# Kernel optimization log

Hardware: AMD Instinct MI355X
Metric: run time of the kernel (lower is better)

The kernel has to match this reference:

```python
import jax, jax.numpy as jnp
import numpy as np

N_WIRES = 8
DIM = 1 << N_WIRES  # 256

# Precompute CNOT permutations (torchquantum convention: wire 0 = MSB)
_idx = np.arange(DIM)
_CNOT_PERMS = []
for _c in range(N_WIRES):
    _t = (_c + 1) % N_WIRES
    _cbit = (_idx >> (N_WIRES - 1 - _c)) & 1
    _CNOT_PERMS.append(np.where(_cbit == 1, _idx ^ (1 << (N_WIRES - 1 - _t)), _idx))
# PauliZ signs per wire: [DIM, N_WIRES]
_ZSIGNS = np.stack([1.0 - 2.0 * ((_idx >> (N_WIRES - 1 - w)) & 1) for w in range(N_WIRES)], axis=1).astype(np.float32)


def _quantum_heads(x, theta):
    """x: [B,S,H,8] angles; theta: [8]. Returns PauliZ expectations [B,S,H,8].

    Simulates per (token,head) an 8-qubit circuit: RX(x_i+theta_i) on wire i
    (encoder RX followed by trainable RX on same wire = one RX with summed angle),
    then CNOT ring 0->1..6->7, 7->0, then MeasureAll PauliZ.
    """
    B, S, H, _ = x.shape
    N = B * S * H
    ang = x.reshape(N, N_WIRES) + theta  # [N,8]
    state = jnp.zeros((N, DIM), dtype=jnp.complex64).at[:, 0].set(1.0)
    half = ang * 0.5
    c_all = jnp.cos(half)
    s_all = jnp.sin(half)
    for w in range(N_WIRES):
        A = 1 << w
        Bdim = 1 << (N_WIRES - 1 - w)
        s = state.reshape(N, A, 2, Bdim)
        a0, a1 = s[:, :, 0, :], s[:, :, 1, :]
        c = c_all[:, w][:, None, None].astype(jnp.complex64)
        isn = (1j * s_all[:, w][:, None, None]).astype(jnp.complex64)
        n0 = c * a0 - isn * a1
        n1 = -isn * a0 + c * a1
        state = jnp.stack([n0, n1], axis=2).reshape(N, DIM)
    for perm in _CNOT_PERMS:
        state = state[:, perm]
    probs = state.real ** 2 + state.imag ** 2  # [N,256]
    exp = probs @ jnp.asarray(_ZSIGNS)  # [N,8]
    return exp.reshape(B, S, H, N_WIRES)


def _mha(proj, W_combine, num_heads):
    # proj: [B,S,E]; q = k = v = proj (identical deterministic projections)
    B, S, E = proj.shape
    d_k = E // num_heads
    qkv = proj.reshape(B, S, num_heads, d_k).transpose(0, 2, 1, 3)  # [B,H,S,dk]
    scores = jnp.einsum('bhqd,bhkd->bhqk', qkv, qkv) / jnp.sqrt(jnp.float32(d_k))
    attn = jax.nn.softmax(scores, axis=-1)
    out = jnp.einsum('bhqk,bhkd->bhqd', attn, qkv)
    out = out.transpose(0, 2, 1, 3).reshape(B, S, E)
    return out @ W_combine.T


def setup_inputs() -> dict:
    key = jax.random.key(0)
    k1, k2, k3 = jax.random.split(key, 3)
    B, S, H = 8, 1024, 8
    E = H * N_WIRES  # 64
    x = jax.random.normal(k1, (B, S, E), dtype=jnp.float32)
    theta = jax.random.normal(k2, (N_WIRES,), dtype=jnp.float32)
    W_combine = jax.random.normal(k3, (E, E), dtype=jnp.float32) * (1.0 / np.sqrt(E))
    return {'x': x, 'theta': theta, 'W_combine': W_combine}


def reference(x, theta, W_combine):
    B, S, E = x.shape
    H = E // N_WIRES
    proj = _quantum_heads(x.reshape(B, S, H, N_WIRES), theta).reshape(B, S, E)
    return _mha(proj, W_combine, H)
```

## Files before the change

kernel.cpp:

```cpp
#include <hip/hip_runtime.h>

typedef _Float16 half4v __attribute__((ext_vector_type(4)));
typedef __fp16 fp16x2 __attribute__((ext_vector_type(2)));
typedef float float4v __attribute__((ext_vector_type(4)));

#define S_ 1024
#define H_ 8
#define B_ 8
#define BH 64
#define NROW 8192
#define E_ 64

#define VST 1032
#define VZOFF (9 * VST)
#define NV (9 * VST + 16)
#define KFZ (64 * 128)
#define NKF (64 * 128 + 8)

static __device__ inline half4v pack4(float a, float b, float c, float d) {
    union { fp16x2 f2[2]; half4v h4; } u;
    u.f2[0] = __builtin_amdgcn_cvt_pkrtz(a, b);
    u.f2[1] = __builtin_amdgcn_cvt_pkrtz(c, d);
    return u.h4;
}

__global__ __launch_bounds__(256, 2) void attn_kernel(
        const float* __restrict__ x, const float* __restrict__ theta,
        _Float16* __restrict__ attnH) {
    __shared__ _Float16 kF[NKF];
    __shared__ _Float16 vT[NV];
    int bh = blockIdx.x;
    int b = bh >> 3, h = bh & 7;
    int tid = threadIdx.x;

    float th[8];
#pragma unroll
    for (int i = 0; i < 8; ++i) th[i] = theta[i];

    {
        const half4v zer = {(_Float16)0.f, (_Float16)0.f, (_Float16)0.f, (_Float16)0.f};
        const half4v one = {(_Float16)1.f, (_Float16)1.f, (_Float16)1.f, (_Float16)1.f};
        if (tid < 4) *(half4v*)&vT[VZOFF + tid * 4] = zer;
        if (tid < 2) *(half4v*)&kF[KFZ + tid * 4] = zer;
        *(half4v*)&vT[8 * VST + tid * 4] = one;
    }

    for (int s = tid; s < S_; s += 256) {
        const float4* xp = (const float4*)(x + (((size_t)(b << 10) + s) << 6) + (h << 3));
        float4 x0 = xp[0];
        float4 x1 = xp[1];
        float c0 = __cosf(x0.x + th[0]);
        float c1 = __cosf(x0.y + th[1]);
        float c2 = __cosf(x0.z + th[2]);
        float c3 = __cosf(x0.w + th[3]);
        float c4 = __cosf(x1.x + th[4]);
        float c5 = __cosf(x1.y + th[5]);
        float c6 = __cosf(x1.z + th[6]);
        float c7 = __cosf(x1.w + th[7]);
        float e1 = c0 * c1;
        float e2 = e1 * c2;
        float e3 = e2 * c3;
        float e4 = e3 * c4;
        float e5 = e4 * c5;
        float e6 = e5 * c6;
        float e7 = e6 * c7;
        float e0 = ((c1 * c2) * (c3 * c4)) * ((c5 * c6) * c7);
        half4v lo = pack4(e0, e1, e2, e3);
        half4v hi = pack4(e4, e5, e6, e7);
        int kt = s >> 4, c = s & 15;
        *(half4v*)&kF[kt * 128 + c * 4]      = lo;
        *(half4v*)&kF[kt * 128 + 64 + c * 4] = hi;
        vT[0 * VST + s] = lo[0]; vT[1 * VST + s] = lo[1];
        vT[2 * VST + s] = lo[2]; vT[3 * VST + s] = lo[3];
        vT[4 * VST + s] = hi[0]; vT[5 * VST + s] = hi[1];
        vT[6 * VST + s] = hi[2]; vT[7 * VST + s] = hi[3];
    }
    __syncthreads();

    int lane = tid & 63;
    int wv   = tid >> 6;
    int col  = lane & 15;
    int quad = lane >> 4;
    int q0   = blockIdx.y * 128 + wv * 32;

    bool lo2 = (quad < 2);

    int kfa = lo2 ? (lane * 4) : KFZ;
    int kstep = lo2 ? 128 : 0;

    half4v qfa = *(const half4v*)&kF[kfa + (q0 >> 4) * kstep];
    half4v qfb = *(const half4v*)&kF[kfa + ((q0 >> 4) + 1) * kstep];
    qfa *= (_Float16)0.51012921f;
    qfb *= (_Float16)0.51012921f;

    int vbase = (col < 9) ? (col * VST + quad * 4) : VZOFF;
    int vstep = (col < 9) ? 16 : 0;

#define LOADK(dst, t) { dst = *(const half4v*)&kF[kfa + (t) * kstep]; }
#define LOADV(dst, t) { dst = *(const half4v*)&vT[vbase + (t) * vstep]; }

    float4v oa = {0.f, 0.f, 0.f, 0.f};
    float4v ob = {0.f, 0.f, 0.f, 0.f};
    const float4v zc = {0.f, 0.f, 0.f, 0.f};
    const float SH = 4.08040428f;

    half4v kA, vA, kB, vB, kN, vN, kM, vM;
    LOADK(kA, 0); LOADV(vA, 0);
    LOADK(kB, 1); LOADV(vB, 1);

    for (int kt = 0; kt < 64; kt += 2) {
        float4v sa = __builtin_amdgcn_mfma_f32_16x16x16f16(kA, qfa, zc, 0, 0, 0);
        float4v sb = __builtin_amdgcn_mfma_f32_16x16x16f16(kA, qfb, zc, 0, 0, 0);
        int t2 = (kt + 2) & 63;
        LOADK(kN, t2); LOADV(vN, t2);
        half4v pa = pack4(__builtin_amdgcn_exp2f(sa[0] - SH),
                          __builtin_amdgcn_exp2f(sa[1] - SH),
                          __builtin_amdgcn_exp2f(sa[2] - SH),
                          __builtin_amdgcn_exp2f(sa[3] - SH));
        half4v pb = pack4(__builtin_amdgcn_exp2f(sb[0] - SH),
                          __builtin_amdgcn_exp2f(sb[1] - SH),
                          __builtin_amdgcn_exp2f(sb[2] - SH),
                          __builtin_amdgcn_exp2f(sb[3] - SH));
        oa = __builtin_amdgcn_mfma_f32_16x16x16f16(vA, pa, oa, 0, 0, 0);
        ob = __builtin_amdgcn_mfma_f32_16x16x16f16(vA, pb, ob, 0, 0, 0);
        float4v sc = __builtin_amdgcn_mfma_f32_16x16x16f16(kB, qfa, zc, 0, 0, 0);
        float4v sd = __builtin_amdgcn_mfma_f32_16x16x16f16(kB, qfb, zc, 0, 0, 0);
        int t3 = (kt + 3) & 63;
        LOADK(kM, t3); LOADV(vM, t3);
        half4v pc = pack4(__builtin_amdgcn_exp2f(sc[0] - SH),
                          __builtin_amdgcn_exp2f(sc[1] - SH),
                          __builtin_amdgcn_exp2f(sc[2] - SH),
                          __builtin_amdgcn_exp2f(sc[3] - SH));
        half4v pd = pack4(__builtin_amdgcn_exp2f(sd[0] - SH),
                          __builtin_amdgcn_exp2f(sd[1] - SH),
                          __builtin_amdgcn_exp2f(sd[2] - SH),
                          __builtin_amdgcn_exp2f(sd[3] - SH));
        oa = __builtin_amdgcn_mfma_f32_16x16x16f16(vB, pc, oa, 0, 0, 0);
        ob = __builtin_amdgcn_mfma_f32_16x16x16f16(vB, pd, ob, 0, 0, 0);
        kA = kN; vA = vN; kB = kM; vB = vM;
    }

    int lsrc = 32 | col;
    {
        float l = __shfl(oa[0], lsrc, 64);
        if (lo2) {
            float inv = __builtin_amdgcn_rcpf(l);
            half4v ov = pack4(oa[0] * inv, oa[1] * inv, oa[2] * inv, oa[3] * inv);
            *(half4v*)(attnH + (((size_t)(b << 10) + q0 + col) << 6) + (h << 3) + quad * 4) = ov;
        }
    }
    {
        float l = __shfl(ob[0], lsrc, 64);
        if (lo2) {
            float inv = __builtin_amdgcn_rcpf(l);
            half4v ov = pack4(ob[0] * inv, ob[1] * inv, ob[2] * inv, ob[3] * inv);
            *(half4v*)(attnH + (((size_t)(b << 10) + q0 + 16 + col) << 6) + (h << 3) + quad * 4) = ov;
        }
    }
#undef LOADK
#undef LOADV
}

__global__ __launch_bounds__(256) void combine_kernel(
        const _Float16* __restrict__ AH, const float* __restrict__ W,
        float* __restrict__ out) {
    __shared__ _Float16 a2[64 * 68];
    __shared__ _Float16 wt[64 * 68];
    int r0 = blockIdx.x * 64;
    int tid = threadIdx.x;

    for (int idx = tid; idx < E_ * E_; idx += 256) {
        int e = idx >> 6, k = idx & 63;
        wt[k * 68 + e] = (_Float16)W[idx];
    }
#pragma unroll
    for (int j = 0; j < 4; ++j) {
        int off = tid * 16 + j * 4;
        int row = off >> 6, k = off & 63;
        *(half4v*)&a2[row * 68 + k] = *(const half4v*)&AH[(size_t)r0 * E_ + off];
    }
    __syncthreads();

    int lane = tid & 63;
    int wv   = tid >> 6;
    int col  = lane & 15;
    int quad = lane >> 4;

    half4v wf[4][4];
#pragma unroll
    for (int t = 0; t < 4; ++t)
#pragma unroll
        for (int e = 0; e < 4; ++e) {
            int kb = (t * 16 + quad * 4) * 68 + e * 16 + col;
            half4v w_ = {wt[kb], wt[kb + 68], wt[kb + 136], wt[kb + 204]};
            wf[t][e] = w_;
        }

    float4v acc[4] = {{0,0,0,0},{0,0,0,0},{0,0,0,0},{0,0,0,0}};
#pragma unroll
    for (int t = 0; t < 4; ++t) {
        half4v af = *(const half4v*)&a2[(wv * 16 + col) * 68 + t * 16 + quad * 4];
#pragma unroll
        for (int e = 0; e < 4; ++e)
            acc[e] = __builtin_amdgcn_mfma_f32_16x16x16f16(af, wf[t][e], acc[e], 0, 0, 0);
    }

#pragma unroll
    for (int e = 0; e < 4; ++e)
#pragma unroll
        for (int r = 0; r < 4; ++r)
            out[(size_t)(r0 + wv * 16 + quad * 4 + r) * E_ + e * 16 + col] = acc[e][r];
}

extern "C" void kernel_launch(void* const* d_in, const int* in_sizes, int n_in,
                              void* d_out, int out_size, void* d_ws, size_t ws_size,
                              hipStream_t stream) {
    const float* x     = (const float*)d_in[0];
    const float* theta = (const float*)d_in[1];
    const float* W     = (const float*)d_in[2];
    float* out = (float*)d_out;

    _Float16* attnH = (_Float16*)d_ws;

    attn_kernel<<<dim3(BH, S_ / 128), 256, 0, stream>>>(x, theta, attnH);
    combine_kernel<<<NROW / 64, 256, 0, stream>>>(attnH, W, out);
}
```

Measured before the change: 74.20 us.

## Halve per-wave query tile, double the grid, and simplify the attention inner loop

Each wave now handles 16 query rows instead of 32, so the attention grid doubles and launch bounds allow 4 blocks per CU, aiming for more waves in flight. The manually software-pipelined two-tile loop becomes a fully unrolled single-accumulator loop. The constant subtraction before exp2 is dropped, relying on the bounded score range to stay within fp16. The zero-padded K and V LDS regions are removed in favour of zeroed query fragments and duplicate V columns whose outputs are discarded. In exchange, every block still recomputes the cosine-product K/V prep for all 1024 keys, so that redundant work doubles.

```diff
diff --git a/kernel.cpp b/kernel.cpp
--- a/kernel.cpp
+++ b/kernel.cpp
@@ -10,12 +10,7 @@
 #define BH 64
 #define NROW 8192
 #define E_ 64
-
 #define VST 1032
-#define VZOFF (9 * VST)
-#define NV (9 * VST + 16)
-#define KFZ (64 * 128)
-#define NKF (64 * 128 + 8)
 
 static __device__ inline half4v pack4(float a, float b, float c, float d) {
     union { fp16x2 f2[2]; half4v h4; } u;
@@ -24,11 +19,11 @@
     return u.h4;
 }
 
-__global__ __launch_bounds__(256, 2) void attn_kernel(
+__global__ __launch_bounds__(256, 4) void attn_kernel(
         const float* __restrict__ x, const float* __restrict__ theta,
         _Float16* __restrict__ attnH) {
-    __shared__ _Float16 kF[NKF];
-    __shared__ _Float16 vT[NV];
+    __shared__ _Float16 kF[64 * 128];
+    __shared__ _Float16 vT[9 * VST];
     int bh = blockIdx.x;
     int b = bh >> 3, h = bh & 7;
     int tid = threadIdx.x;
@@ -38,10 +33,7 @@
     for (int i = 0; i < 8; ++i) th[i] = theta[i];
 
     {
-        const half4v zer = {(_Float16)0.f, (_Float16)0.f, (_Float16)0.f, (_Float16)0.f};
         const half4v one = {(_Float16)1.f, (_Float16)1.f, (_Float16)1.f, (_Float16)1.f};
-        if (tid < 4) *(half4v*)&vT[VZOFF + tid * 4] = zer;
-        if (tid < 2) *(half4v*)&kF[KFZ + tid * 4] = zer;
         *(half4v*)&vT[8 * VST + tid * 4] = one;
     }
 
@@ -81,84 +73,39 @@
     int wv   = tid >> 6;
     int col  = lane & 15;
     int quad = lane >> 4;
-    int q0   = blockIdx.y * 128 + wv * 32;
+    int q0   = blockIdx.y * 64 + wv * 16;
 
     bool lo2 = (quad < 2);
 
-    int kfa = lo2 ? (lane * 4) : KFZ;
-    int kstep = lo2 ? 128 : 0;
+    int kbase = (lane & 31) * 4;
+    int vcol = (col < 9) ? col : (col - 8);
+    int vbase = vcol * VST + quad * 4;
 
-    half4v qfa = *(const half4v*)&kF[kfa + (q0 >> 4) * kstep];
-    half4v qfb = *(const half4v*)&kF[kfa + ((q0 >> 4) + 1) * kstep];
-    qfa *= (_Float16)0.51012921f;
-    qfb *= (_Float16)0.51012921f;
+    half4v qf = {(_Float16)0.f, (_Float16)0.f, (_Float16)0.f, (_Float16)0.f};
+    if (lo2) qf = *(const half4v*)&kF[kbase + (q0 >> 4) * 128];
+    qf *= (_Float16)0.51012921f;
 
-    int vbase = (col < 9) ? (col * VST + quad * 4) : VZOFF;
-    int vstep = (col < 9) ? 16 : 0;
+    float4v oacc = {0.f, 0.f, 0.f, 0.f};
+    const float4v zc = {0.f, 0.f, 0.f, 0.f};
 
-#define LOADK(dst, t) { dst = *(const half4v*)&kF[kfa + (t) * kstep]; }
-#define LOADV(dst, t) { dst = *(const half4v*)&vT[vbase + (t) * vstep]; }
-
-    float4v oa = {0.f, 0.f, 0.f, 0.f};
-    float4v ob = {0.f, 0.f, 0.f, 0.f};
-    const float4v zc = {0.f, 0.f, 0.f, 0.f};
-    const float SH = 4.08040428f;
-
-    half4v kA, vA, kB, vB, kN, vN, kM, vM;
-    LOADK(kA, 0); LOADV(vA, 0);
-    LOADK(kB, 1); LOADV(vB, 1);
-
-    for (int kt = 0; kt < 64; kt += 2) {
-        float4v sa = __builtin_amdgcn_mfma_f32_16x16x16f16(kA, qfa, zc, 0, 0, 0);
-        float4v sb = __builtin_amdgcn_mfma_f32_16x16x16f16(kA, qfb, zc, 0, 0, 0);
-        int t2 = (kt + 2) & 63;
-        LOADK(kN, t2); LOADV(vN, t2);
-        half4v pa = pack4(__builtin_amdgcn_exp2f(sa[0] - SH),
-                          __builtin_amdgcn_exp2f(sa[1] - SH),
-                          __builtin_amdgcn_exp2f(sa[2] - SH),
-                          __builtin_amdgcn_exp2f(sa[3] - SH));
-        half4v pb = pack4(__builtin_amdgcn_exp2f(sb[0] - SH),
-                          __builtin_amdgcn_exp2f(sb[1] - SH),
-                          __builtin_amdgcn_exp2f(sb[2] - SH),
-                          __builtin_amdgcn_exp2f(sb[3] - SH));
-        oa = __builtin_amdgcn_mfma_f32_16x16x16f16(vA, pa, oa, 0, 0, 0);
-        ob = __builtin_amdgcn_mfma_f32_16x16x16f16(vA, pb, ob, 0, 0, 0);
-        float4v sc = __builtin_amdgcn_mfma_f32_16x16x16f16(kB, qfa, zc, 0, 0, 0);
-        float4v sd = __builtin_amdgcn_mfma_f32_16x16x16f16(kB, qfb, zc, 0, 0, 0);
-        int t3 = (kt + 3) & 63;
-        LOADK(kM, t3); LOADV(vM, t3);
-        half4v pc = pack4(__builtin_amdgcn_exp2f(sc[0] - SH),
-                          __builtin_amdgcn_exp2f(sc[1] - SH),
-                          __builtin_amdgcn_exp2f(sc[2] - SH),
-                          __builtin_amdgcn_exp2f(sc[3] - SH));
-        half4v pd = pack4(__builtin_amdgcn_exp2f(sd[0] - SH),
-                          __builtin_amdgcn_exp2f(sd[1] - SH),
-                          __builtin_amdgcn_exp2f(sd[2] - SH),
-                          __builtin_amdgcn_exp2f(sd[3] - SH));
-        oa = __builtin_amdgcn_mfma_f32_16x16x16f16(vB, pc, oa, 0, 0, 0);
-        ob = __builtin_amdgcn_mfma_f32_16x16x16f16(vB, pd, ob, 0, 0, 0);
-        kA = kN; vA = vN; kB = kM; vB = vM;
+#pragma unroll
+    for (int kt = 0; kt < 64; ++kt) {
+        half4v kf = *(const half4v*)&kF[kbase + kt * 128];
+        half4v vf = *(const half4v*)&vT[vbase + kt * 16];
+        float4v st = __builtin_amdgcn_mfma_f32_16x16x16f16(kf, qf, zc, 0, 0, 0);
+        half4v pf = pack4(__builtin_amdgcn_exp2f(st[0]),
+                          __builtin_amdgcn_exp2f(st[1]),
+                          __builtin_amdgcn_exp2f(st[2]),
+                          __builtin_amdgcn_exp2f(st[3]));
+        oacc = __builtin_amdgcn_mfma_f32_16x16x16f16(vf, pf, oacc, 0, 0, 0);
     }
 
-    int lsrc = 32 | col;
-    {
-        float l = __shfl(oa[0], lsrc, 64);
-        if (lo2) {
-            float inv = __builtin_amdgcn_rcpf(l);
-            half4v ov = pack4(oa[0] * inv, oa[1] * inv, oa[2] * inv, oa[3] * inv);
-            *(half4v*)(attnH + (((size_t)(b << 10) + q0 + col) << 6) + (h << 3) + quad * 4) = ov;
-        }
+    float l = __shfl(oacc[0], 32 | col, 64);
+    if (lo2) {
+        float inv = __builtin_amdgcn_rcpf(l);
+        half4v ov = pack4(oacc[0] * inv, oacc[1] * inv, oacc[2] * inv, oacc[3] * inv);
+        *(half4v*)(attnH + (((size_t)(b << 10) + q0 + col) << 6) + (h << 3) + quad * 4) = ov;
     }
-    {
-        float l = __shfl(ob[0], lsrc, 64);
-        if (lo2) {
-            float inv = __builtin_amdgcn_rcpf(l);
-            half4v ov = pack4(ob[0] * inv, ob[1] * inv, ob[2] * inv, ob[3] * inv);
-            *(half4v*)(attnH + (((size_t)(b << 10) + q0 + 16 + col) << 6) + (h << 3) + quad * 4) = ov;
-        }
-    }
-#undef LOADK
-#undef LOADV
 }
 
 __global__ __launch_bounds__(256) void combine_kernel(
@@ -222,6 +169,6 @@
 
     _Float16* attnH = (_Float16*)d_ws;
 
-    attn_kernel<<<dim3(BH, S_ / 128), 256, 0, stream>>>(x, theta, attnH);
+    attn_kernel<<<dim3(BH, S_ / 64), 256, 0, stream>>>(x, theta, attnH);
     combine_kernel<<<NROW / 64, 256, 0, stream>>>(attnH, W, out);
 }
```

Measured after the change: 73.65 us. Within noise of the previous version (-0.7%).
